# Kernel tuning notes

Hardware: AMD Instinct MI355X
Metric: run time of the kernel (lower is better)

The kernel has to match this reference:

```python
import jax, jax.numpy as jnp
import numpy as np

B, T, C = 4, 4096, 1024
ATT_SCALE = 1.0
TIME_MIX_RATIO = 1.0


def setup_inputs() -> dict:
    key = jax.random.key(0)
    ks = jax.random.split(key, 7)
    std = 0.02  # 0.02 * (layer_id + 1), layer_id = 0
    x = jax.random.normal(ks[0], (B, T, C), dtype=jnp.float32)
    state = jnp.zeros((B, C), dtype=jnp.float32)
    W_r = jax.random.normal(ks[1], (C, C), dtype=jnp.float32) * std
    W_k = jax.random.normal(ks[2], (C, C), dtype=jnp.float32) * std
    W_v = jax.random.normal(ks[3], (C, C), dtype=jnp.float32) * std
    W_o = jax.random.normal(ks[4], (C, C), dtype=jnp.float32) * std
    time_mix_r = jnp.ones((1, 1, C), dtype=jnp.float32) * TIME_MIX_RATIO
    time_mix_k = jnp.ones((1, 1, C), dtype=jnp.float32) * TIME_MIX_RATIO
    time_mix_v = jnp.ones((1, 1, C), dtype=jnp.float32) * TIME_MIX_RATIO
    # learned log-decay; use negative values so exp(time_decay) < 1 and the
    # recurrence is numerically stable over T=4096 steps (a trained model
    # would have such values; the torch init 0.9 would blow up for long T)
    time_decay = jax.random.uniform(ks[5], (C,), dtype=jnp.float32,
                                    minval=-0.1, maxval=-0.01)
    return {"x": x, "state": state, "W_r": W_r, "W_k": W_k, "W_v": W_v,
            "W_o": W_o, "time_mix_r": time_mix_r, "time_mix_k": time_mix_k,
            "time_mix_v": time_mix_v, "time_decay": time_decay}


def reference(x, state, W_r, W_k, W_v, W_o,
              time_mix_r, time_mix_k, time_mix_v, time_decay):
    # shifted input: previous-token stream, seeded with incoming state
    x_mix = jnp.concatenate([state[:, None, :], x[:, :-1]], axis=1)  # [B,T,C]

    r_in = x * time_mix_r + x_mix * (1.0 - time_mix_r)
    k_in = x * time_mix_k + x_mix * (1.0 - time_mix_k)
    v_in = x * time_mix_v + x_mix * (1.0 - time_mix_v)

    r = jax.nn.sigmoid(jnp.einsum('btc,dc->btd', r_in, W_r))
    k = jnp.exp(jnp.einsum('btc,dc->btd', k_in, W_k))
    v = jnp.einsum('btc,dc->btd', v_in, W_v)

    decay = jnp.exp(time_decay)  # [C]
    kv = k * v                   # [B,T,C]

    def step(s, inp):
        kv_t, r_t = inp          # each [B,C]
        s = s * decay + kv_t
        return s, r_t * s

    _, out = jax.lax.scan(step, state,
                          (kv.transpose(1, 0, 2), r.transpose(1, 0, 2)))
    out = out.transpose(1, 0, 2) * ATT_SCALE          # [B,T,C]

    output = jnp.einsum('btc,dc->btd', out, W_o)      # time_output
    new_state = x[:, -1]
    return output, new_state
```

## Files before the change

### kernel.cpp

```cpp
#include <hip/hip_runtime.h>

#define B_ 4
#define T_ 4096
#define C_ 1024
#define M_ (B_*T_)
#define BTC (B_*T_*C_)
#define NCHUNK 64
#define CHUNK (T_ / NCHUNK)

typedef unsigned short u16;
typedef __attribute__((ext_vector_type(8))) short bf16x8;
typedef __attribute__((ext_vector_type(8))) unsigned short u16x8;
typedef __attribute__((ext_vector_type(4))) float f32x4;
typedef __attribute__((ext_vector_type(16))) float f32x16;

static __device__ __forceinline__ u16 f2bf(float f) {
    unsigned u = __float_as_uint(f);
    unsigned r = (u + 0x7FFFu + ((u >> 16) & 1u)) >> 16;
    return (u16)r;
}
static __device__ __forceinline__ float bf2f(u16 h) {
    return __uint_as_float(((unsigned)h) << 16);
}

__global__ void prep_kernel(const float* __restrict__ x, const float* __restrict__ state,
                            const float* __restrict__ tmr, const float* __restrict__ tmk,
                            const float* __restrict__ tmv,
                            u16* __restrict__ rin, u16* __restrict__ kin, u16* __restrict__ vin,
                            float* __restrict__ new_state) {
    const int idx = blockIdx.x * 256 + threadIdx.x;
    const int c8 = idx & 127;
    const int bt = idx >> 7;
    const int t  = bt & (T_ - 1);
    const int b  = bt >> 12;

    const float4* xv = (const float4*)x;
    float4 xa = xv[idx * 2], xb = xv[idx * 2 + 1];
    float4 pa, pb;
    if (t == 0) {
        const float4* sv = (const float4*)state;
        pa = sv[(b * 128 + c8) * 2]; pb = sv[(b * 128 + c8) * 2 + 1];
    } else {
        pa = xv[(idx - 128) * 2]; pb = xv[(idx - 128) * 2 + 1];
    }
    float4 mra = ((const float4*)tmr)[c8 * 2], mrb = ((const float4*)tmr)[c8 * 2 + 1];
    float4 mka = ((const float4*)tmk)[c8 * 2], mkb = ((const float4*)tmk)[c8 * 2 + 1];
    float4 mva = ((const float4*)tmv)[c8 * 2], mvb = ((const float4*)tmv)[c8 * 2 + 1];

    float xc[8] = {xa.x, xa.y, xa.z, xa.w, xb.x, xb.y, xb.z, xb.w};
    float xp[8] = {pa.x, pa.y, pa.z, pa.w, pb.x, pb.y, pb.z, pb.w};
    float mr[8] = {mra.x, mra.y, mra.z, mra.w, mrb.x, mrb.y, mrb.z, mrb.w};
    float mk[8] = {mka.x, mka.y, mka.z, mka.w, mkb.x, mkb.y, mkb.z, mkb.w};
    float mv[8] = {mva.x, mva.y, mva.z, mva.w, mvb.x, mvb.y, mvb.z, mvb.w};

    u16x8 pr, pk, pv;
#pragma unroll
    for (int j = 0; j < 8; ++j) {
        pr[j] = f2bf(xc[j] * mr[j] + xp[j] * (1.f - mr[j]));
        pk[j] = f2bf(xc[j] * mk[j] + xp[j] * (1.f - mk[j]));
        pv[j] = f2bf(xc[j] * mv[j] + xp[j] * (1.f - mv[j]));
    }
    ((u16x8*)rin)[idx] = pr;
    ((u16x8*)kin)[idx] = pk;
    ((u16x8*)vin)[idx] = pv;
    if (t == T_ - 1) {
        ((float4*)new_state)[(b * 128 + c8) * 2]     = xa;
        ((float4*)new_state)[(b * 128 + c8) * 2 + 1] = xb;
    }
}

__global__ void cast_all_kernel(const float* __restrict__ w0, const float* __restrict__ w1,
                                const float* __restrict__ w2, const float* __restrict__ w3,
                                u16* __restrict__ dst) {
    int w = blockIdx.x >> 10;
    int i = ((blockIdx.x & 1023) << 8) + threadIdx.x;
    const float* src = (w == 0) ? w0 : (w == 1) ? w1 : (w == 2) ? w2 : w3;
    float4 v = ((const float4*)src)[i];
    ushort4 o;
    o.x = f2bf(v.x); o.y = f2bf(v.y); o.z = f2bf(v.z); o.w = f2bf(v.w);
    ((ushort4*)(dst + (size_t)w * C_ * C_))[i] = o;
}

#define EPI_SIG  0
#define EPI_EXP  1
#define EPI_BF16 2
#define EPI_F32  3

__global__ __launch_bounds__(512, 2)
void gemm256(const u16* __restrict__ A0, const u16* __restrict__ A1, const u16* __restrict__ A2,
             const u16* __restrict__ Wb, void* __restrict__ C0, void* __restrict__ C1,
             void* __restrict__ C2, int epis) {
    extern __shared__ __align__(16) u16 smem[];
    u16* sA = smem;
    u16* sB = smem + 2 * 256 * 64;

    const int id = blockIdx.x >> 8;
    const int wg = blockIdx.x & 255;
    const u16* A = (id == 0) ? A0 : (id == 1) ? A1 : A2;
    const u16* W = Wb + (size_t)id * C_ * C_;
    void* Cptr   = (id == 0) ? C0 : (id == 1) ? C1 : C2;
    const int epi = (epis >> (id * 8)) & 255;

    const int tid  = threadIdx.x;
    const int wid  = tid >> 6, lane = tid & 63;
    const int wr   = wid >> 2, wc = wid & 3;
    const int l31  = lane & 31, kh = lane >> 5;

    const int wgid = (wg & 7) * 32 + (wg >> 3);
    const int bm   = wgid >> 2, bn = wgid & 3;
    const int row0 = bm * 256, col0 = bn * 256;
    const int K    = C_;
    const int nk   = K / 64;

    f32x16 acc[4][2];
#pragma unroll
    for (int i = 0; i < 4; ++i)
#pragma unroll
        for (int j = 0; j < 2; ++j)
#pragma unroll
            for (int q = 0; q < 16; ++q) acc[i][j][q] = 0.f;

    const int rl = tid >> 3;
    const int uu = tid & 7;
    const int usw = uu ^ (rl & 7);

    auto stA = [&](int buf, int h, int kt) {
#pragma unroll
        for (int p = 0; p < 2; ++p) {
            int rt = h * 128 + p * 64 + rl;
            const u16* g = A + (size_t)(row0 + rt) * K + kt * 64 + usw * 8;
            __builtin_amdgcn_global_load_lds(
                (const __attribute__((address_space(1))) void*)g,
                (__attribute__((address_space(3))) void*)&sA[buf * 16384 + rt * 64 + uu * 8],
                16, 0, 0);
        }
    };
    auto stB = [&](int buf, int h, int kt) {
#pragma unroll
        for (int p = 0; p < 2; ++p) {
            int rt = h * 128 + p * 64 + rl;
            const u16* g = W + (size_t)(col0 + rt) * K + kt * 64 + usw * 8;
            __builtin_amdgcn_global_load_lds(
                (const __attribute__((address_space(1))) void*)g,
                (__attribute__((address_space(3))) void*)&sB[buf * 16384 + rt * 64 + uu * 8],
                16, 0, 0);
        }
    };
    auto ldA = [&](int buf, int rt, int ks) -> bf16x8 {
        int R = wr * 128 + rt * 32 + l31;
        int unit = (ks * 2 + kh) ^ (l31 & 7);
        return *(const bf16x8*)&sA[buf * 16384 + R * 64 + unit * 8];
    };
    auto ldB = [&](int buf, int ct, int ks) -> bf16x8 {
        int R = wc * 64 + ct * 32 + l31;
        int unit = (ks * 2 + kh) ^ (l31 & 7);
        return *(const bf16x8*)&sB[buf * 16384 + R * 64 + unit * 8];
    };

    stA(0, 0, 0); stA(0, 1, 0); stB(0, 0, 0); stB(0, 1, 0);
    stB(1, 0, 1); stB(1, 1, 1);
    asm volatile("s_waitcnt vmcnt(4)" ::: "memory");
    __builtin_amdgcn_s_barrier();

    for (int kt = 0; kt < nk; ++kt) {
        const int cur = kt & 1, nxt = cur ^ 1;
        const int t1 = (kt + 1 < nk) ? kt + 1 : nk - 1;
        const int t2 = (kt + 2 < nk) ? kt + 2 : nk - 1;

        bf16x8 b[2][4];
        {
            bf16x8 a[4];
#pragma unroll
            for (int ct = 0; ct < 2; ++ct)
#pragma unroll
                for (int ks = 0; ks < 4; ++ks) b[ct][ks] = ldB(cur, ct, ks);
#pragma unroll
            for (int ks = 0; ks < 4; ++ks) a[ks] = ldA(cur, 0, ks);
            stA(nxt, 0, t1);
            __builtin_amdgcn_sched_barrier(0);
            __builtin_amdgcn_s_setprio(1);
#pragma unroll
            for (int ks = 0; ks < 4; ++ks)
#pragma unroll
                for (int ct = 0; ct < 2; ++ct)
                    acc[0][ct] = __builtin_amdgcn_mfma_f32_32x32x16_bf16(a[ks], b[ct][ks], acc[0][ct], 0, 0, 0);
            __builtin_amdgcn_s_setprio(0);
            __builtin_amdgcn_s_barrier();
        }
        {
            bf16x8 a[4];
#pragma unroll
            for (int ks = 0; ks < 4; ++ks) a[ks] = ldA(cur, 1, ks);
            stA(nxt, 1, t1);
            __builtin_amdgcn_sched_barrier(0);
            __builtin_amdgcn_s_setprio(1);
#pragma unroll
            for (int ks = 0; ks < 4; ++ks)
#pragma unroll
                for (int ct = 0; ct < 2; ++ct)
                    acc[1][ct] = __builtin_amdgcn_mfma_f32_32x32x16_bf16(a[ks], b[ct][ks], acc[1][ct], 0, 0, 0);
            __builtin_amdgcn_s_setprio(0);
            __builtin_amdgcn_s_barrier();
        }
        {
            bf16x8 a[4];
#pragma unroll
            for (int ks = 0; ks < 4; ++ks) a[ks] = ldA(cur, 2, ks);
            stB(cur, 0, t2);
            __builtin_amdgcn_sched_barrier(0);
            __builtin_amdgcn_s_setprio(1);
#pragma unroll
            for (int ks = 0; ks < 4; ++ks)
#pragma unroll
                for (int ct = 0; ct < 2; ++ct)
                    acc[2][ct] = __builtin_amdgcn_mfma_f32_32x32x16_bf16(a[ks], b[ct][ks], acc[2][ct], 0, 0, 0);
            __builtin_amdgcn_s_setprio(0);
            __builtin_amdgcn_s_barrier();
        }
        {
            bf16x8 a[4];
#pragma unroll
            for (int ks = 0; ks < 4; ++ks) a[ks] = ldA(cur, 3, ks);
            stB(cur, 1, t2);
            __builtin_amdgcn_sched_barrier(0);
            __builtin_amdgcn_s_setprio(1);
#pragma unroll
            for (int ks = 0; ks < 4; ++ks)
#pragma unroll
                for (int ct = 0; ct < 2; ++ct)
                    acc[3][ct] = __builtin_amdgcn_mfma_f32_32x32x16_bf16(a[ks], b[ct][ks], acc[3][ct], 0, 0, 0);
            __builtin_amdgcn_s_setprio(0);
            asm volatile("s_waitcnt vmcnt(4)" ::: "memory");
            __builtin_amdgcn_s_barrier();
        }
    }

    const int r0 = row0 + wr * 128;
    const int c0 = col0 + wc * 64;
#pragma unroll
    for (int rt = 0; rt < 4; ++rt) {
#pragma unroll
        for (int ct = 0; ct < 2; ++ct) {
#pragma unroll
            for (int q = 0; q < 16; ++q) {
                int rr = r0 + rt * 32 + (q & 3) + 8 * (q >> 2) + 4 * kh;
                int cc = c0 + ct * 32 + l31;
                float v = acc[rt][ct][q];
                size_t o = (size_t)rr * C_ + cc;
                if (epi == EPI_SIG) {
                    ((u16*)Cptr)[o] = f2bf(1.0f / (1.0f + __expf(-v)));
                } else if (epi == EPI_EXP) {
                    ((u16*)Cptr)[o] = f2bf(__expf(v));
                } else if (epi == EPI_BF16) {
                    ((u16*)Cptr)[o] = f2bf(v);
                } else {
                    ((float*)Cptr)[o] = v;
                }
            }
        }
    }
}

__global__ void scan_partial(const u16* __restrict__ ek, const u16* __restrict__ vv,
                             const float* __restrict__ td, float* __restrict__ S) {
    const int tid = threadIdx.x;
    const int bid = blockIdx.x;
    const int ct  = bid & 3;
    const int j   = (bid >> 2) & (NCHUNK - 1);
    const int b   = bid >> 8;
    const int c   = ct * 256 + tid;
    const float d = __expf(td[c]);
    float s = 0.f;
    size_t base = ((size_t)(b * T_ + j * CHUNK)) * C_ + c;
#pragma unroll 4
    for (int t = 0; t < CHUNK; ++t) {
        size_t ix = base + (size_t)t * C_;
        s = s * d + bf2f(ek[ix]) * bf2f(vv[ix]);
    }
    S[((size_t)(b * NCHUNK + j)) * C_ + c] = s;
}

__global__ void scan_carry(const float* __restrict__ S, const float* __restrict__ td,
                           const float* __restrict__ state, float* __restrict__ carry) {
    int id = blockIdx.x * blockDim.x + threadIdx.x;
    if (id >= B_ * C_) return;
    int c = id & (C_ - 1);
    int b = id >> 10;
    float dl = __expf(td[c] * (float)CHUNK);
    float E = state[id];
#pragma unroll 8
    for (int j = 0; j < NCHUNK; ++j) {
        size_t o = ((size_t)(b * NCHUNK + j)) * C_ + c;
        carry[o] = E;
        E = dl * E + S[o];
    }
}

__global__ void scan_apply(const u16* __restrict__ ek, const u16* __restrict__ vv,
                           const u16* __restrict__ rr, const float* __restrict__ td,
                           const float* __restrict__ carry, u16* __restrict__ out) {
    const int tid = threadIdx.x;
    const int bid = blockIdx.x;
    const int ct  = bid & 3;
    const int j   = (bid >> 2) & (NCHUNK - 1);
    const int b   = bid >> 8;
    const int c   = ct * 256 + tid;
    const float d = __expf(td[c]);
    float s = carry[((size_t)(b * NCHUNK + j)) * C_ + c];
    size_t base = ((size_t)(b * T_ + j * CHUNK)) * C_ + c;
#pragma unroll 4
    for (int t = 0; t < CHUNK; ++t) {
        size_t ix = base + (size_t)t * C_;
        s = s * d + bf2f(ek[ix]) * bf2f(vv[ix]);
        out[ix] = f2bf(s * bf2f(rr[ix]));
    }
}

extern "C" void kernel_launch(void* const* d_in, const int* in_sizes, int n_in,
                              void* d_out, int out_size, void* d_ws, size_t ws_size,
                              hipStream_t stream) {
    const float* x     = (const float*)d_in[0];
    const float* state = (const float*)d_in[1];
    const float* W_r   = (const float*)d_in[2];
    const float* W_k   = (const float*)d_in[3];
    const float* W_v   = (const float*)d_in[4];
    const float* W_o   = (const float*)d_in[5];
    const float* tmr   = (const float*)d_in[6];
    const float* tmk   = (const float*)d_in[7];
    const float* tmv   = (const float*)d_in[8];
    const float* td    = (const float*)d_in[9];

    float* out_f     = (float*)d_out;
    float* new_state = out_f + (size_t)BTC;

    char* ws = (char*)d_ws;
    const size_t SZ = (size_t)BTC * 2;
    u16* rin   = (u16*)(ws + 0 * SZ);
    u16* kin   = (u16*)(ws + 1 * SZ);
    u16* vin   = (u16*)(ws + 2 * SZ);
    u16* rbuf  = (u16*)(ws + 3 * SZ);
    u16* ekbuf = (u16*)(ws + 4 * SZ);
    u16* vbuf  = (u16*)(ws + 5 * SZ);
    u16* wts   = (u16*)(ws + 6 * SZ);
    u16* wrb   = wts;
    u16* wob   = wts + 3 * (size_t)C_ * C_;
    float* Sbuf  = (float*)(wob + (size_t)C_ * C_);
    float* cbuf  = Sbuf + (size_t)B_ * NCHUNK * C_;
    u16* outb  = vin;

    prep_kernel<<<BTC / 8 / 256, 256, 0, stream>>>(
        x, state, tmr, tmk, tmv, rin, kin, vin, new_state);

    cast_all_kernel<<<4096, 256, 0, stream>>>(W_r, W_k, W_v, W_o, wts);

    const int LDSB = 2 * 2 * 256 * 64 * 2;
    const int epis3 = EPI_SIG | (EPI_EXP << 8) | (EPI_BF16 << 16);
    gemm256<<<768, 512, LDSB, stream>>>(rin, kin, vin, wrb,
                                        (void*)rbuf, (void*)ekbuf, (void*)vbuf, epis3);

    const int nscan_blocks = B_ * NCHUNK * (C_ / 256);
    scan_partial<<<nscan_blocks, 256, 0, stream>>>(ekbuf, vbuf, td, Sbuf);
    scan_carry<<<(B_ * C_ + 255) / 256, 256, 0, stream>>>(Sbuf, td, state, cbuf);
    scan_apply<<<nscan_blocks, 256, 0, stream>>>(ekbuf, vbuf, rbuf, td, cbuf, outb);

    gemm256<<<256, 512, LDSB, stream>>>(outb, outb, outb, wob,
                                        (void*)out_f, (void*)out_f, (void*)out_f, EPI_F32);
}
```

Before: 266.9 us.

## Switch GEMM to 16x16x32 MFMA with triple-buffered A tiles and template epilogues

The GEMM kernel now uses 16x16x32 bf16 MFMA instead of 32x32x16, with a 3-stage ring for A tiles in LDS (5 tiles total) and an extra barrier plus lgkmcnt wait per sub-step. Epilogues are compile-time template parameters and write 4-wide vectors instead of scalar stores. The single fused 768-block launch for r/k/v is split into three 256-block launches. The intent is to remove runtime epilogue branching, widen stores, and deepen prefetch, at the cost of more LDS (fewer blocks per CU), extra barriers, and the loss of concurrency from the combined launch.

Result: faster. 250.9 us (-6.0%).

```diff
diff --git a/kernel.cpp b/kernel.cpp
--- a/kernel.cpp
+++ b/kernel.cpp
@@ -12,7 +12,6 @@
 typedef __attribute__((ext_vector_type(8))) short bf16x8;
 typedef __attribute__((ext_vector_type(8))) unsigned short u16x8;
 typedef __attribute__((ext_vector_type(4))) float f32x4;
-typedef __attribute__((ext_vector_type(16))) float f32x16;
 
 static __device__ __forceinline__ u16 f2bf(float f) {
     unsigned u = __float_as_uint(f);
@@ -86,39 +85,33 @@
 #define EPI_BF16 2
 #define EPI_F32  3
 
+template <int EPI>
 __global__ __launch_bounds__(512, 2)
-void gemm256(const u16* __restrict__ A0, const u16* __restrict__ A1, const u16* __restrict__ A2,
-             const u16* __restrict__ Wb, void* __restrict__ C0, void* __restrict__ C1,
-             void* __restrict__ C2, int epis) {
+void gemm256(const u16* __restrict__ A, const u16* __restrict__ W, void* __restrict__ Cptr) {
     extern __shared__ __align__(16) u16 smem[];
     u16* sA = smem;
-    u16* sB = smem + 2 * 256 * 64;
-
-    const int id = blockIdx.x >> 8;
-    const int wg = blockIdx.x & 255;
-    const u16* A = (id == 0) ? A0 : (id == 1) ? A1 : A2;
-    const u16* W = Wb + (size_t)id * C_ * C_;
-    void* Cptr   = (id == 0) ? C0 : (id == 1) ? C1 : C2;
-    const int epi = (epis >> (id * 8)) & 255;
+    u16* sB = smem + 3 * 16384;
+
+    const int N = C_, K = C_;
+    const int nk = K / 64;
 
     const int tid  = threadIdx.x;
     const int wid  = tid >> 6, lane = tid & 63;
     const int wr   = wid >> 2, wc = wid & 3;
-    const int l31  = lane & 31, kh = lane >> 5;
-
+    const int lr   = lane & 15, kq = lane >> 4;
+
+    const int wg   = blockIdx.x;
     const int wgid = (wg & 7) * 32 + (wg >> 3);
     const int bm   = wgid >> 2, bn = wgid & 3;
     const int row0 = bm * 256, col0 = bn * 256;
-    const int K    = C_;
-    const int nk   = K / 64;
-
-    f32x16 acc[4][2];
-#pragma unroll
-    for (int i = 0; i < 4; ++i)
-#pragma unroll
-        for (int j = 0; j < 2; ++j)
-#pragma unroll
-            for (int q = 0; q < 16; ++q) acc[i][j][q] = 0.f;
+
+    f32x4 acc[8][4];
+#pragma unroll
+    for (int i = 0; i < 8; ++i)
+#pragma unroll
+        for (int j = 0; j < 4; ++j)
+#pragma unroll
+            for (int q = 0; q < 4; ++q) acc[i][j][q] = 0.f;
 
     const int rl = tid >> 3;
     const int uu = tid & 7;
@@ -146,91 +139,115 @@
                 16, 0, 0);
         }
     };
-    auto ldA = [&](int buf, int rt, int ks) -> bf16x8 {
-        int R = wr * 128 + rt * 32 + l31;
-        int unit = (ks * 2 + kh) ^ (l31 & 7);
+    auto ldA = [&](int buf, int ig, int ks) -> bf16x8 {
+        int R = wr * 128 + ig * 16 + lr;
+        int unit = (ks * 4 + kq) ^ (lr & 7);
         return *(const bf16x8*)&sA[buf * 16384 + R * 64 + unit * 8];
     };
-    auto ldB = [&](int buf, int ct, int ks) -> bf16x8 {
-        int R = wc * 64 + ct * 32 + l31;
-        int unit = (ks * 2 + kh) ^ (l31 & 7);
+    auto ldB = [&](int buf, int j, int ks) -> bf16x8 {
+        int R = wc * 64 + j * 16 + lr;
+        int unit = (ks * 4 + kq) ^ (lr & 7);
         return *(const bf16x8*)&sB[buf * 16384 + R * 64 + unit * 8];
     };
 
     stA(0, 0, 0); stA(0, 1, 0); stB(0, 0, 0); stB(0, 1, 0);
-    stB(1, 0, 1); stB(1, 1, 1);
-    asm volatile("s_waitcnt vmcnt(4)" ::: "memory");
+    stA(1, 0, 1); stA(1, 1, 1); stB(1, 0, 1); stB(1, 1, 1);
+    asm volatile("s_waitcnt vmcnt(8)" ::: "memory");
     __builtin_amdgcn_s_barrier();
 
     for (int kt = 0; kt < nk; ++kt) {
-        const int cur = kt & 1, nxt = cur ^ 1;
-        const int t1 = (kt + 1 < nk) ? kt + 1 : nk - 1;
-        const int t2 = (kt + 2 < nk) ? kt + 2 : nk - 1;
-
-        bf16x8 b[2][4];
+        const int curA = kt % 3, curB = kt & 1;
+        const int dstA = (kt + 2) % 3;
+        const int t2   = (kt + 2 < nk) ? kt + 2 : nk - 1;
+
+        bf16x8 b[4][2];
         {
-            bf16x8 a[4];
-#pragma unroll
-            for (int ct = 0; ct < 2; ++ct)
-#pragma unroll
-                for (int ks = 0; ks < 4; ++ks) b[ct][ks] = ldB(cur, ct, ks);
-#pragma unroll
-            for (int ks = 0; ks < 4; ++ks) a[ks] = ldA(cur, 0, ks);
-            stA(nxt, 0, t1);
+            bf16x8 a[2][2];
+#pragma unroll
+            for (int j = 0; j < 4; ++j)
+#pragma unroll
+                for (int ks = 0; ks < 2; ++ks) b[j][ks] = ldB(curB, j, ks);
+#pragma unroll
+            for (int i = 0; i < 2; ++i)
+#pragma unroll
+                for (int ks = 0; ks < 2; ++ks) a[i][ks] = ldA(curA, i, ks);
+            stA(dstA, 0, t2);
+            __builtin_amdgcn_s_barrier();
+            asm volatile("s_waitcnt lgkmcnt(0)" ::: "memory");
             __builtin_amdgcn_sched_barrier(0);
             __builtin_amdgcn_s_setprio(1);
 #pragma unroll
-            for (int ks = 0; ks < 4; ++ks)
-#pragma unroll
-                for (int ct = 0; ct < 2; ++ct)
-                    acc[0][ct] = __builtin_amdgcn_mfma_f32_32x32x16_bf16(a[ks], b[ct][ks], acc[0][ct], 0, 0, 0);
+            for (int i = 0; i < 2; ++i)
+#pragma unroll
+                for (int j = 0; j < 4; ++j)
+#pragma unroll
+                    for (int ks = 0; ks < 2; ++ks)
+                        acc[i][j] = __builtin_amdgcn_mfma_f32_16x16x32_bf16(b[j][ks], a[i][ks], acc[i][j], 0, 0, 0);
             __builtin_amdgcn_s_setprio(0);
             __builtin_amdgcn_s_barrier();
         }
         {
-            bf16x8 a[4];
-#pragma unroll
-            for (int ks = 0; ks < 4; ++ks) a[ks] = ldA(cur, 1, ks);
-            stA(nxt, 1, t1);
+            bf16x8 a[2][2];
+#pragma unroll
+            for (int i = 0; i < 2; ++i)
+#pragma unroll
+                for (int ks = 0; ks < 2; ++ks) a[i][ks] = ldA(curA, 2 + i, ks);
+            stA(dstA, 1, t2);
+            __builtin_amdgcn_s_barrier();
+            asm volatile("s_waitcnt lgkmcnt(0)" ::: "memory");
             __builtin_amdgcn_sched_barrier(0);
             __builtin_amdgcn_s_setprio(1);
 #pragma unroll
-            for (int ks = 0; ks < 4; ++ks)
-#pragma unroll
-                for (int ct = 0; ct < 2; ++ct)
-                    acc[1][ct] = __builtin_amdgcn_mfma_f32_32x32x16_bf16(a[ks], b[ct][ks], acc[1][ct], 0, 0, 0);
+            for (int i = 0; i < 2; ++i)
+#pragma unroll
+                for (int j = 0; j < 4; ++j)
+#pragma unroll
+                    for (int ks = 0; ks < 2; ++ks)
+                        acc[2 + i][j] = __builtin_amdgcn_mfma_f32_16x16x32_bf16(b[j][ks], a[i][ks], acc[2 + i][j], 0, 0, 0);
             __builtin_amdgcn_s_setprio(0);
             __builtin_amdgcn_s_barrier();
         }
         {
-            bf16x8 a[4];
-#pragma unroll
-            for (int ks = 0; ks < 4; ++ks) a[ks] = ldA(cur, 2, ks);
-            stB(cur, 0, t2);
+            bf16x8 a[2][2];
+#pragma unroll
+            for (int i = 0; i < 2; ++i)
+#pragma unroll
+                for (int ks = 0; ks < 2; ++ks) a[i][ks] = ldA(curA, 4 + i, ks);
+            stB(curB, 0, t2);
+            __builtin_amdgcn_s_barrier();
+            asm volatile("s_waitcnt lgkmcnt(0)" ::: "memory");
             __builtin_amdgcn_sched_barrier(0);
             __builtin_amdgcn_s_setprio(1);
 #pragma unroll
-            for (int ks = 0; ks < 4; ++ks)
-#pragma unroll
-                for (int ct = 0; ct < 2; ++ct)
-                    acc[2][ct] = __builtin_amdgcn_mfma_f32_32x32x16_bf16(a[ks], b[ct][ks], acc[2][ct], 0, 0, 0);
+            for (int i = 0; i < 2; ++i)
+#pragma unroll
+                for (int j = 0; j < 4; ++j)
+#pragma unroll
+                    for (int ks = 0; ks < 2; ++ks)
+                        acc[4 + i][j] = __builtin_amdgcn_mfma_f32_16x16x32_bf16(b[j][ks], a[i][ks], acc[4 + i][j], 0, 0, 0);
             __builtin_amdgcn_s_setprio(0);
             __builtin_amdgcn_s_barrier();
         }
         {
-            bf16x8 a[4];
-#pragma unroll
-            for (int ks = 0; ks < 4; ++ks) a[ks] = ldA(cur, 3, ks);
-            stB(cur, 1, t2);
+            bf16x8 a[2][2];
+#pragma unroll
+            for (int i = 0; i < 2; ++i)
+#pragma unroll
+                for (int ks = 0; ks < 2; ++ks) a[i][ks] = ldA(curA, 6 + i, ks);
+            stB(curB, 1, t2);
+            __builtin_amdgcn_s_barrier();
+            asm volatile("s_waitcnt lgkmcnt(0)" ::: "memory");
             __builtin_amdgcn_sched_barrier(0);
             __builtin_amdgcn_s_setprio(1);
 #pragma unroll
-            for (int ks = 0; ks < 4; ++ks)
-#pragma unroll
-                for (int ct = 0; ct < 2; ++ct)
-                    acc[3][ct] = __builtin_amdgcn_mfma_f32_32x32x16_bf16(a[ks], b[ct][ks], acc[3][ct], 0, 0, 0);
+            for (int i = 0; i < 2; ++i)
+#pragma unroll
+                for (int j = 0; j < 4; ++j)
+#pragma unroll
+                    for (int ks = 0; ks < 2; ++ks)
+                        acc[6 + i][j] = __builtin_amdgcn_mfma_f32_16x16x32_bf16(b[j][ks], a[i][ks], acc[6 + i][j], 0, 0, 0);
             __builtin_amdgcn_s_setprio(0);
-            asm volatile("s_waitcnt vmcnt(4)" ::: "memory");
+            asm volatile("s_waitcnt vmcnt(8)" ::: "memory");
             __builtin_amdgcn_s_barrier();
         }
     }
@@ -238,24 +255,30 @@
     const int r0 = row0 + wr * 128;
     const int c0 = col0 + wc * 64;
 #pragma unroll
-    for (int rt = 0; rt < 4; ++rt) {
-#pragma unroll
-        for (int ct = 0; ct < 2; ++ct) {
-#pragma unroll
-            for (int q = 0; q < 16; ++q) {
-                int rr = r0 + rt * 32 + (q & 3) + 8 * (q >> 2) + 4 * kh;
-                int cc = c0 + ct * 32 + l31;
-                float v = acc[rt][ct][q];
-                size_t o = (size_t)rr * C_ + cc;
-                if (epi == EPI_SIG) {
-                    ((u16*)Cptr)[o] = f2bf(1.0f / (1.0f + __expf(-v)));
-                } else if (epi == EPI_EXP) {
-                    ((u16*)Cptr)[o] = f2bf(__expf(v));
-                } else if (epi == EPI_BF16) {
-                    ((u16*)Cptr)[o] = f2bf(v);
+    for (int i = 0; i < 8; ++i) {
+        const int rr = r0 + i * 16 + lr;
+#pragma unroll
+        for (int j = 0; j < 4; ++j) {
+            const int cc = c0 + j * 16 + kq * 4;
+            f32x4 v = acc[i][j];
+            if constexpr (EPI == EPI_F32) {
+                float4 o = {v[0], v[1], v[2], v[3]};
+                *(float4*)((float*)Cptr + (size_t)rr * N + cc) = o;
+            } else {
+                ushort4 o;
+                if constexpr (EPI == EPI_SIG) {
+                    o.x = f2bf(1.0f / (1.0f + __expf(-v[0])));
+                    o.y = f2bf(1.0f / (1.0f + __expf(-v[1])));
+                    o.z = f2bf(1.0f / (1.0f + __expf(-v[2])));
+                    o.w = f2bf(1.0f / (1.0f + __expf(-v[3])));
+                } else if constexpr (EPI == EPI_EXP) {
+                    o.x = f2bf(__expf(v[0])); o.y = f2bf(__expf(v[1]));
+                    o.z = f2bf(__expf(v[2])); o.w = f2bf(__expf(v[3]));
                 } else {
-                    ((float*)Cptr)[o] = v;
+                    o.x = f2bf(v[0]); o.y = f2bf(v[1]);
+                    o.z = f2bf(v[2]); o.w = f2bf(v[3]);
                 }
+                *(ushort4*)((u16*)Cptr + (size_t)rr * N + cc) = o;
             }
         }
     }
@@ -343,26 +366,32 @@
     u16* vbuf  = (u16*)(ws + 5 * SZ);
     u16* wts   = (u16*)(ws + 6 * SZ);
     u16* wrb   = wts;
-    u16* wob   = wts + 3 * (size_t)C_ * C_;
+    u16* wkb   = wrb + (size_t)C_ * C_;
+    u16* wvb   = wkb + (size_t)C_ * C_;
+    u16* wob   = wvb + (size_t)C_ * C_;
     float* Sbuf  = (float*)(wob + (size_t)C_ * C_);
     float* cbuf  = Sbuf + (size_t)B_ * NCHUNK * C_;
     u16* outb  = vin;
 
+    const int LDSB = 5 * 16384 * 2;
+    (void)hipFuncSetAttribute((const void*)gemm256<EPI_SIG>,  hipFuncAttributeMaxDynamicSharedMemorySize, LDSB);
+    (void)hipFuncSetAttribute((const void*)gemm256<EPI_EXP>,  hipFuncAttributeMaxDynamicSharedMemorySize, LDSB);
+    (void)hipFuncSetAttribute((const void*)gemm256<EPI_BF16>, hipFuncAttributeMaxDynamicSharedMemorySize, LDSB);
+    (void)hipFuncSetAttribute((const void*)gemm256<EPI_F32>,  hipFuncAttributeMaxDynamicSharedMemorySize, LDSB);
+
     prep_kernel<<<BTC / 8 / 256, 256, 0, stream>>>(
         x, state, tmr, tmk, tmv, rin, kin, vin, new_state);
 
     cast_all_kernel<<<4096, 256, 0, stream>>>(W_r, W_k, W_v, W_o, wts);
 
-    const int LDSB = 2 * 2 * 256 * 64 * 2;
-    const int epis3 = EPI_SIG | (EPI_EXP << 8) | (EPI_BF16 << 16);
-    gemm256<<<768, 512, LDSB, stream>>>(rin, kin, vin, wrb,
-                                        (void*)rbuf, (void*)ekbuf, (void*)vbuf, epis3);
+    gemm256<EPI_SIG ><<<256, 512, LDSB, stream>>>(rin, wrb, (void*)rbuf);
+    gemm256<EPI_EXP ><<<256, 512, LDSB, stream>>>(kin, wkb, (void*)ekbuf);
+    gemm256<EPI_BF16><<<256, 512, LDSB, stream>>>(vin, wvb, (void*)vbuf);
 
     const int nscan_blocks = B_ * NCHUNK * (C_ / 256);
     scan_partial<<<nscan_blocks, 256, 0, stream>>>(ekbuf, vbuf, td, Sbuf);
     scan_carry<<<(B_ * C_ + 255) / 256, 256, 0, stream>>>(Sbuf, td, state, cbuf);
     scan_apply<<<nscan_blocks, 256, 0, stream>>>(ekbuf, vbuf, rbuf, td, cbuf, outb);
 
-    gemm256<<<256, 512, LDSB, stream>>>(outb, outb, outb, wob,
-                                        (void*)out_f, (void*)out_f, (void*)out_f, EPI_F32);
-}
+    gemm256<EPI_F32><<<256, 512, LDSB, stream>>>(outb, wob, (void*)out_f);
+}
```
